# Optimization experiments

Hardware: AMD Instinct MI355X
Metric: run time of the kernel (lower is better)

## Reference

```python
import jax, jax.numpy as jnp
import numpy as np

HIDDEN = 640
ATTN_DIM = 128
LN_EPS = 1e-5


def setup_inputs() -> dict:
    key = jax.random.key(0)
    ks = jax.random.split(key, 5)
    B, N = 16, 20000
    gene_hiddens = jax.random.normal(ks[0], (B, N, HIDDEN), dtype=jnp.float32)
    gene_pos_repr = jax.random.normal(ks[1], (B, HIDDEN), dtype=jnp.float32)
    Wq = 0.02 * jax.random.normal(ks[2], (ATTN_DIM, HIDDEN), dtype=jnp.float32)
    Wk = 0.02 * jax.random.normal(ks[3], (ATTN_DIM, HIDDEN), dtype=jnp.float32)
    # v_proj initialized as identity in the torch module; perturb slightly to keep it generic
    Wv = jnp.eye(HIDDEN, dtype=jnp.float32) + 0.01 * jax.random.normal(ks[4], (HIDDEN, HIDDEN), dtype=jnp.float32)
    ln_gamma = jnp.ones((HIDDEN,), dtype=jnp.float32)
    ln_beta = jnp.zeros((HIDDEN,), dtype=jnp.float32)
    return {"gene_hiddens": gene_hiddens, "gene_pos_repr": gene_pos_repr,
            "Wq": Wq, "Wk": Wk, "Wv": Wv, "ln_gamma": ln_gamma, "ln_beta": ln_beta}


def _layer_norm(x, gamma, beta):
    mu = jnp.mean(x, axis=-1, keepdims=True)
    var = jnp.mean(jnp.square(x - mu), axis=-1, keepdims=True)
    return (x - mu) * jax.lax.rsqrt(var + LN_EPS) * gamma + beta


def reference(gene_hiddens, gene_pos_repr, Wq, Wk, Wv, ln_gamma, ln_beta):
    scale = ATTN_DIM ** (-0.5)
    q = gene_pos_repr @ Wq.T                       # [B, A]
    k = jnp.einsum('bnh,ah->bna', gene_hiddens, Wk)  # [B, N, A]
    scores = jnp.einsum('ba,bna->bn', q, k) * scale  # [B, N]
    attn = jax.nn.softmax(scores, axis=-1)           # [B, N]
    v = jnp.einsum('bnh,vh->bnv', gene_hiddens, Wv)  # [B, N, H]
    pooled = jnp.einsum('bn,bnv->bv', attn, v)       # [B, H]
    return _layer_norm(pooled, ln_gamma, ln_beta)
```

## Files before the change

kernel.cpp:

```cpp
#include <hip/hip_runtime.h>
#include <math.h>

#define B 16
#define N 20000
#define H 640
#define A 128
#define LN_EPS 1e-5f
#define SCALE 0.08838834764831843f

__global__ __launch_bounds__(256) void qk_kernel(
    const float* __restrict__ pos, const float* __restrict__ Wq,
    const float* __restrict__ Wk, float* __restrict__ qk) {
  int b = blockIdx.x;
  __shared__ float sp[H];
  __shared__ float sq[A];
  for (int i = threadIdx.x; i < H; i += 256) sp[i] = pos[b * H + i];
  __syncthreads();
  if (threadIdx.x < A) {
    int a = threadIdx.x;
    const float* wr = Wq + (size_t)a * H;
    float acc = 0.f;
    for (int h = 0; h < H; h++) acc += wr[h] * sp[h];
    sq[a] = acc;
  }
  __syncthreads();
  for (int h = threadIdx.x; h < H; h += 256) {
    float acc = 0.f;
    for (int a = 0; a < A; a++) acc += Wk[(size_t)a * H + h] * sq[a];
    qk[b * H + h] = acc * SCALE;
  }
}

__global__ __launch_bounds__(256) void pass1_kernel(
    const float* __restrict__ gh, const float* __restrict__ qk,
    float* __restrict__ pm, float* __restrict__ pl, float* __restrict__ po,
    int blocks_per_b) {
  int b = blockIdx.x / blocks_per_b;
  int blk = blockIdx.x - b * blocks_per_b;
  int wid = threadIdx.x >> 6;
  int lane = threadIdx.x & 63;
  int w = blk * 4 + wid;
  int nw = blocks_per_b * 4;

  const float2* qk2 = (const float2*)(qk + b * H);
  float2 qv[5];
#pragma unroll
  for (int k = 0; k < 5; k++) qv[k] = qk2[lane + 64 * k];

  const float2* ghb = (const float2*)(gh + (size_t)b * N * H);
  float m = -INFINITY, l = 0.f;
  float o[10];
#pragma unroll
  for (int k = 0; k < 10; k++) o[k] = 0.f;

  for (int n = w; n < N; n += nw) {
    const float2* row = ghb + (size_t)n * (H / 2);
    float2 hv[5];
#pragma unroll
    for (int k = 0; k < 5; k++) hv[k] = row[lane + 64 * k];
    float dot = 0.f;
#pragma unroll
    for (int k = 0; k < 5; k++) dot += hv[k].x * qv[k].x + hv[k].y * qv[k].y;
#pragma unroll
    for (int off = 32; off >= 1; off >>= 1) dot += __shfl_xor(dot, off);
    float mn = fmaxf(m, dot);
    float alpha = __expf(m - mn);
    float wt = __expf(dot - mn);
    l = l * alpha + wt;
#pragma unroll
    for (int k = 0; k < 5; k++) {
      o[2 * k]     = o[2 * k] * alpha     + wt * hv[k].x;
      o[2 * k + 1] = o[2 * k + 1] * alpha + wt * hv[k].y;
    }
    m = mn;
  }

  __shared__ float wm[4], wl[4];
  __shared__ float wo[4][H];
  if (lane == 0) { wm[wid] = m; wl[wid] = l; }
#pragma unroll
  for (int k = 0; k < 5; k++) {
    wo[wid][2 * lane + 128 * k]     = o[2 * k];
    wo[wid][2 * lane + 128 * k + 1] = o[2 * k + 1];
  }
  __syncthreads();
  float M = fmaxf(fmaxf(wm[0], wm[1]), fmaxf(wm[2], wm[3]));
  float e0 = __expf(wm[0] - M), e1 = __expf(wm[1] - M);
  float e2 = __expf(wm[2] - M), e3 = __expf(wm[3] - M);
  int idx = b * blocks_per_b + blk;
  for (int e = threadIdx.x; e < H; e += 256) {
    po[(size_t)idx * H + e] =
        wo[0][e] * e0 + wo[1][e] * e1 + wo[2][e] * e2 + wo[3][e] * e3;
  }
  if (threadIdx.x == 0) {
    pm[idx] = M;
    pl[idx] = wl[0] * e0 + wl[1] * e1 + wl[2] * e2 + wl[3] * e3;
  }
}

__device__ __forceinline__ float block_reduce_640(float v, float* red) {
  int lane = threadIdx.x & 63, wid = threadIdx.x >> 6;
#pragma unroll
  for (int off = 32; off >= 1; off >>= 1) v += __shfl_xor(v, off);
  __syncthreads();
  if (lane == 0) red[wid] = v;
  __syncthreads();
  float t = 0.f;
#pragma unroll
  for (int j = 0; j < 10; j++) t += red[j];
  return t;
}

__global__ __launch_bounds__(640) void finalize_kernel(
    const float* __restrict__ pm, const float* __restrict__ pl,
    const float* __restrict__ po, const float* __restrict__ Wv,
    const float* __restrict__ gamma, const float* __restrict__ beta,
    float* __restrict__ out, int blocks_per_b) {
  int b = blockIdx.x;
  int tid = threadIdx.x;
  __shared__ float sh[H];
  __shared__ float red[16];

  float M = -INFINITY;
  for (int j = 0; j < blocks_per_b; j++) M = fmaxf(M, pm[b * blocks_per_b + j]);
  float L = 0.f;
  for (int j = 0; j < blocks_per_b; j++)
    L += pl[b * blocks_per_b + j] * __expf(pm[b * blocks_per_b + j] - M);
  float invL = 1.f / L;

  float s = 0.f;
  for (int j = 0; j < blocks_per_b; j++) {
    s += po[(size_t)(b * blocks_per_b + j) * H + tid] *
         __expf(pm[b * blocks_per_b + j] - M);
  }
  sh[tid] = s * invL;
  __syncthreads();

  const float* wrow = Wv + (size_t)tid * H;
  float acc = 0.f;
  for (int h = 0; h < H; h++) acc += wrow[h] * sh[h];

  float mu = block_reduce_640(acc, red) * (1.f / H);
  float d = acc - mu;
  float var = block_reduce_640(d * d, red) * (1.f / H);
  out[b * H + tid] = d * rsqrtf(var + LN_EPS) * gamma[tid] + beta[tid];
}

extern "C" void kernel_launch(void* const* d_in, const int* in_sizes, int n_in,
                              void* d_out, int out_size, void* d_ws, size_t ws_size,
                              hipStream_t stream) {
  const float* gh    = (const float*)d_in[0];
  const float* pos   = (const float*)d_in[1];
  const float* Wq    = (const float*)d_in[2];
  const float* Wk    = (const float*)d_in[3];
  const float* Wv    = (const float*)d_in[4];
  const float* gamma = (const float*)d_in[5];
  const float* beta  = (const float*)d_in[6];
  float* out = (float*)d_out;
  float* ws = (float*)d_ws;

  int blocks_per_b = 64;
  while (blocks_per_b > 1 &&
         (size_t)(B * H + 2 * B * 64 + B * blocks_per_b * H) * 4 > ws_size)
    blocks_per_b >>= 1;

  float* qk = ws;
  float* pm = ws + B * H;
  float* pl = pm + B * 64;
  float* po = pl + B * 64;

  qk_kernel<<<B, 256, 0, stream>>>(pos, Wq, Wk, qk);
  pass1_kernel<<<B * blocks_per_b, 256, 0, stream>>>(gh, qk, pm, pl, po,
                                                     blocks_per_b);
  finalize_kernel<<<B, 640, 0, stream>>>(pm, pl, po, Wv, gamma, beta, out,
                                         blocks_per_b);
}
```

Measured before the change: 1.130 ms.

## Coalesce weight GEMVs and process row pairs per wave with lazy softmax rescale

The Wq and Wv matrix-vector products now assign one row per wave and read each row in coalesced float2 chunks followed by a wave reduction, replacing the old one-row-per-thread strided reads. In the main streaming pass, each wave splits into two 32-lane halves that each handle one row, so every iteration loads two rows with float4 loads. The online-softmax rescale of the accumulator is skipped when the running max does not increase. The partial sums from the two halves are combined with a cross-half shuffle before the block reduction, which adds some shuffle work and more registers per thread.

```diff
diff --git a/kernel.cpp b/kernel.cpp
--- a/kernel.cpp
+++ b/kernel.cpp
@@ -12,19 +12,33 @@
     const float* __restrict__ pos, const float* __restrict__ Wq,
     const float* __restrict__ Wk, float* __restrict__ qk) {
   int b = blockIdx.x;
+  int tid = threadIdx.x;
+  int wid = tid >> 6, lane = tid & 63;
   __shared__ float sp[H];
   __shared__ float sq[A];
-  for (int i = threadIdx.x; i < H; i += 256) sp[i] = pos[b * H + i];
-  __syncthreads();
-  if (threadIdx.x < A) {
-    int a = threadIdx.x;
-    const float* wr = Wq + (size_t)a * H;
-    float acc = 0.f;
-    for (int h = 0; h < H; h++) acc += wr[h] * sp[h];
-    sq[a] = acc;
-  }
-  __syncthreads();
-  for (int h = threadIdx.x; h < H; h += 256) {
+  for (int i = tid; i < H; i += 256) sp[i] = pos[b * H + i];
+  __syncthreads();
+
+  float2 spf[5];
+  const float2* sp2 = (const float2*)sp;
+#pragma unroll
+  for (int k = 0; k < 5; k++) spf[k] = sp2[lane + 64 * k];
+  for (int j = 0; j < 32; j++) {
+    int a = wid * 32 + j;
+    const float2* wr = (const float2*)(Wq + (size_t)a * H);
+    float dot = 0.f;
+#pragma unroll
+    for (int k = 0; k < 5; k++) {
+      float2 v = wr[lane + 64 * k];
+      dot += v.x * spf[k].x + v.y * spf[k].y;
+    }
+#pragma unroll
+    for (int off = 32; off >= 1; off >>= 1) dot += __shfl_xor(dot, off);
+    if (lane == 0) sq[a] = dot;
+  }
+  __syncthreads();
+
+  for (int h = tid; h < H; h += 256) {
     float acc = 0.f;
     for (int a = 0; a < A; a++) acc += Wk[(size_t)a * H + h] * sq[a];
     qk[b * H + h] = acc * SCALE;
@@ -39,58 +53,88 @@
   int blk = blockIdx.x - b * blocks_per_b;
   int wid = threadIdx.x >> 6;
   int lane = threadIdx.x & 63;
+  int half = lane >> 5;
+  int li = lane & 31;
   int w = blk * 4 + wid;
   int nw = blocks_per_b * 4;
-
-  const float2* qk2 = (const float2*)(qk + b * H);
-  float2 qv[5];
-#pragma unroll
-  for (int k = 0; k < 5; k++) qv[k] = qk2[lane + 64 * k];
-
-  const float2* ghb = (const float2*)(gh + (size_t)b * N * H);
+  int npairs = N / 2;
+
+  const float4* qk4 = (const float4*)(qk + b * H);
+  float4 qv[5];
+#pragma unroll
+  for (int k = 0; k < 5; k++) qv[k] = qk4[li + 32 * k];
+
+  const float* ghb = gh + (size_t)b * N * H;
   float m = -INFINITY, l = 0.f;
-  float o[10];
-#pragma unroll
-  for (int k = 0; k < 10; k++) o[k] = 0.f;
-
-  for (int n = w; n < N; n += nw) {
-    const float2* row = ghb + (size_t)n * (H / 2);
-    float2 hv[5];
-#pragma unroll
-    for (int k = 0; k < 5; k++) hv[k] = row[lane + 64 * k];
+  float4 o[5];
+#pragma unroll
+  for (int k = 0; k < 5; k++) o[k] = make_float4(0.f, 0.f, 0.f, 0.f);
+
+  for (int p = w; p < npairs; p += nw) {
+    const float4* row = (const float4*)(ghb + (size_t)(2 * p + half) * H);
+    float4 hv[5];
+#pragma unroll
+    for (int k = 0; k < 5; k++) hv[k] = row[li + 32 * k];
     float dot = 0.f;
 #pragma unroll
-    for (int k = 0; k < 5; k++) dot += hv[k].x * qv[k].x + hv[k].y * qv[k].y;
-#pragma unroll
-    for (int off = 32; off >= 1; off >>= 1) dot += __shfl_xor(dot, off);
-    float mn = fmaxf(m, dot);
-    float alpha = __expf(m - mn);
-    float wt = __expf(dot - mn);
-    l = l * alpha + wt;
-#pragma unroll
     for (int k = 0; k < 5; k++) {
-      o[2 * k]     = o[2 * k] * alpha     + wt * hv[k].x;
-      o[2 * k + 1] = o[2 * k + 1] * alpha + wt * hv[k].y;
-    }
-    m = mn;
+      dot += hv[k].x * qv[k].x + hv[k].y * qv[k].y +
+             hv[k].z * qv[k].z + hv[k].w * qv[k].w;
+    }
+#pragma unroll
+    for (int off = 16; off >= 1; off >>= 1) dot += __shfl_xor(dot, off);
+    float sA = __shfl(dot, 0);
+    float sB = __shfl(dot, 32);
+    float smax = fmaxf(sA, sB);
+    if (smax <= m) {
+      float wtA = __expf(sA - m), wtB = __expf(sB - m);
+      l += wtA + wtB;
+      float wt = half ? wtB : wtA;
+#pragma unroll
+      for (int k = 0; k < 5; k++) {
+        o[k].x += wt * hv[k].x; o[k].y += wt * hv[k].y;
+        o[k].z += wt * hv[k].z; o[k].w += wt * hv[k].w;
+      }
+    } else {
+      float alpha = __expf(m - smax);
+      float wtA = __expf(sA - smax), wtB = __expf(sB - smax);
+      l = l * alpha + wtA + wtB;
+      float wt = half ? wtB : wtA;
+#pragma unroll
+      for (int k = 0; k < 5; k++) {
+        o[k].x = o[k].x * alpha + wt * hv[k].x;
+        o[k].y = o[k].y * alpha + wt * hv[k].y;
+        o[k].z = o[k].z * alpha + wt * hv[k].z;
+        o[k].w = o[k].w * alpha + wt * hv[k].w;
+      }
+      m = smax;
+    }
+  }
+
+#pragma unroll
+  for (int k = 0; k < 5; k++) {
+    o[k].x += __shfl_xor(o[k].x, 32);
+    o[k].y += __shfl_xor(o[k].y, 32);
+    o[k].z += __shfl_xor(o[k].z, 32);
+    o[k].w += __shfl_xor(o[k].w, 32);
   }
 
   __shared__ float wm[4], wl[4];
-  __shared__ float wo[4][H];
+  __shared__ float4 wo4[4][H / 4];
   if (lane == 0) { wm[wid] = m; wl[wid] = l; }
-#pragma unroll
-  for (int k = 0; k < 5; k++) {
-    wo[wid][2 * lane + 128 * k]     = o[2 * k];
-    wo[wid][2 * lane + 128 * k + 1] = o[2 * k + 1];
+  if (half == 0) {
+#pragma unroll
+    for (int k = 0; k < 5; k++) wo4[wid][li + 32 * k] = o[k];
   }
   __syncthreads();
   float M = fmaxf(fmaxf(wm[0], wm[1]), fmaxf(wm[2], wm[3]));
   float e0 = __expf(wm[0] - M), e1 = __expf(wm[1] - M);
   float e2 = __expf(wm[2] - M), e3 = __expf(wm[3] - M);
+  const float* wof = (const float*)wo4;
   int idx = b * blocks_per_b + blk;
   for (int e = threadIdx.x; e < H; e += 256) {
-    po[(size_t)idx * H + e] =
-        wo[0][e] * e0 + wo[1][e] * e1 + wo[2][e] * e2 + wo[3][e] * e3;
+    po[(size_t)idx * H + e] = wof[e] * e0 + wof[H + e] * e1 +
+                              wof[2 * H + e] * e2 + wof[3 * H + e] * e3;
   }
   if (threadIdx.x == 0) {
     pm[idx] = M;
@@ -118,7 +162,9 @@
     float* __restrict__ out, int blocks_per_b) {
   int b = blockIdx.x;
   int tid = threadIdx.x;
+  int wid = tid >> 6, lane = tid & 63;
   __shared__ float sh[H];
+  __shared__ float pooled[H];
   __shared__ float red[16];
 
   float M = -INFINITY;
@@ -136,10 +182,26 @@
   sh[tid] = s * invL;
   __syncthreads();
 
-  const float* wrow = Wv + (size_t)tid * H;
-  float acc = 0.f;
-  for (int h = 0; h < H; h++) acc += wrow[h] * sh[h];
-
+  float2 shf[5];
+  const float2* sh2 = (const float2*)sh;
+#pragma unroll
+  for (int k = 0; k < 5; k++) shf[k] = sh2[lane + 64 * k];
+  for (int j = 0; j < 64; j++) {
+    int r = wid * 64 + j;
+    const float2* wr = (const float2*)(Wv + (size_t)r * H);
+    float dot = 0.f;
+#pragma unroll
+    for (int k = 0; k < 5; k++) {
+      float2 v = wr[lane + 64 * k];
+      dot += v.x * shf[k].x + v.y * shf[k].y;
+    }
+#pragma unroll
+    for (int off = 32; off >= 1; off >>= 1) dot += __shfl_xor(dot, off);
+    if (lane == 0) pooled[r] = dot;
+  }
+  __syncthreads();
+
+  float acc = pooled[tid];
   float mu = block_reduce_640(acc, red) * (1.f / H);
   float d = acc - mu;
   float var = block_reduce_640(d * d, red) * (1.f / H);
```

Measured after the change: 1.131 ms. No clear change (+0.1%).
